# Kernel optimization log

Measured on AMD Instinct MI355X. Metric: run time of the kernel, lower is better.

The kernel has to match this reference:

```python
import jax, jax.numpy as jnp
import numpy as np


def setup_inputs() -> dict:
    key = jax.random.key(0)
    k1, k2, k3, k4, k5 = jax.random.split(key, 5)
    B, L, G, DG = 2, 8192, 256, 8
    D = G * DG
    x1 = jax.random.normal(k1, (B, L, G, DG), dtype=jnp.float32)
    x2 = jax.random.normal(k2, (B, L, G, DG), dtype=jnp.float32)
    v = jax.random.normal(k3, (B, L, G, DG), dtype=jnp.float32)
    # implicit/explicit filter output: one length-L kernel per group, scaled down
    # like a decaying long-conv filter so outputs stay O(1)
    t = jnp.arange(L, dtype=jnp.float32)
    decay = jnp.exp(-t / 1024.0)[None, :]  # (1, L)
    h = jax.random.normal(k4, (G, L), dtype=jnp.float32) * decay / jnp.sqrt(jnp.float32(L))
    conv_bias = jax.random.normal(k5, (D,), dtype=jnp.float32)
    return {"x1": x1, "x2": x2, "v": v, "h": h, "conv_bias": conv_bias}


def reference(x1, x2, v, h, conv_bias):
    # x1, x2, v: (B, L, G, DG); h: (G, L); conv_bias: (G*DG,)
    B, L, G, DG = x1.shape
    D = G * DG
    # 'b l g dg -> b (g dg) l'
    x1c = x1.reshape(B, L, D).transpose(0, 2, 1)  # (B, D, L)
    x2c = x2.reshape(B, L, D).transpose(0, 2, 1)
    vc = v.reshape(B, L, D).transpose(0, 2, 1)

    kv = x2c * vc  # pre-gate: (B, D, L)

    fft_size = 2 * L  # causal (linear) convolution via zero-padded FFT
    # each group's filter is shared across its DG channels
    h_rep = jnp.repeat(h, DG, axis=0)  # (D, L)
    kv_f = jnp.fft.rfft(kv.astype(jnp.float32), n=fft_size)
    h_f = jnp.fft.rfft(h_rep.astype(jnp.float32), n=fft_size)
    y = jnp.fft.irfft(kv_f * h_f[None], n=fft_size)[..., :L]  # (B, D, L)

    y = y + kv * conv_bias[None, :, None]  # skip/bias term
    z = x1c * y  # post-gate (identity gating activation)

    # back to (B, L, D)
    return z.transpose(0, 2, 1)
```

## Files before the change

kernel.cpp:

```cpp
#include <hip/hip_runtime.h>
#include <hip/hip_bf16.h>

typedef __attribute__((ext_vector_type(8))) __bf16 bf16x8;
typedef __attribute__((ext_vector_type(4))) __bf16 bf16x4;
typedef __attribute__((ext_vector_type(4))) float  f32x4;

#define L_LEN   8192
#define D_DIM   2048
#define G_NUM   256
#define HP      8320
#define HS      808
#define KVS     264

__global__ __launch_bounds__(256) void prep_kv_kernel(
    const float* __restrict__ x2, const float* __restrict__ v,
    __bf16* __restrict__ kvout)
{
  __shared__ __bf16 sT[128 * 64];
  const int tid = threadIdx.x;
  const int l0 = blockIdx.x << 7;
  const int d0 = blockIdx.y << 6;
  const int b  = blockIdx.z;
  const int lr = tid >> 4;
  const int dq = tid & 15;
#pragma unroll
  for (int p = 0; p < 8; ++p) {
    const int ll = (p << 4) + lr;
    const size_t idx = ((size_t)(b * L_LEN + l0 + ll)) * D_DIM + d0 + (dq << 2);
    const f32x4 a = *(const f32x4*)&x2[idx];
    const f32x4 c = *(const f32x4*)&v[idx];
    bf16x4 kvv;
    kvv[0] = (__bf16)(a[0] * c[0]);
    kvv[1] = (__bf16)(a[1] * c[1]);
    kvv[2] = (__bf16)(a[2] * c[2]);
    kvv[3] = (__bf16)(a[3] * c[3]);
    *(bf16x4*)&sT[(ll << 6) + (((dq ^ (ll >> 3)) & 15) << 2)] = kvv;
  }
  __syncthreads();
#pragma unroll
  for (int p = 0; p < 2; ++p) {
    const int c  = tid + (p << 8);
    const int r  = c >> 3, seg = c & 7;
    const int rb = r >> 2, rl = r & 3;
    const int gch = d0 + r;
    const int row = ((gch >> 3) << 4) + (b << 3) + (gch & 7);
    bf16x8 w0, w1;
#pragma unroll
    for (int j = 0; j < 8; ++j) {
      const int lj0 = (seg << 4) + j;
      const int lj1 = lj0 + 8;
      w0[j] = sT[(lj0 << 6) + (((rb ^ (lj0 >> 3)) & 15) << 2) + rl];
      w1[j] = sT[(lj1 << 6) + (((rb ^ (lj1 >> 3)) & 15) << 2) + rl];
    }
    __bf16* dst = kvout + (size_t)row * L_LEN + l0 + (seg << 4);
    *(bf16x8*)dst = w0;
    *(bf16x8*)(dst + 8) = w1;
  }
}

__global__ __launch_bounds__(256) void prep_h_kernel(
    const float* __restrict__ h, __bf16* __restrict__ hr)
{
  const unsigned i = blockIdx.x * 256u + threadIdx.x;
  const unsigned g = i / (8u * HP);
  const unsigned r = i - g * (8u * HP);
  const unsigned s = r / HP;
  const unsigned z = r - s * HP;
  const int P = 8255 - (int)z - (int)s;
  __bf16 val = (__bf16)0.0f;
  if (P >= 0 && P < 8192) val = (__bf16)h[(size_t)g * 8192 + P];
  hr[i] = val;
}

__global__ __launch_bounds__(256, 3) void conv_kernel(
    const __bf16* __restrict__ KV, const __bf16* __restrict__ HR,
    const float* __restrict__ x1, const float* __restrict__ bias,
    float* __restrict__ out)
{
  __shared__ __bf16 sKV[2][16 * KVS];
  __shared__ __bf16 sH[2][8 * HS];

  const int g   = blockIdx.x;
  const int jb  = 15 - (int)blockIdx.y;
  const int l0  = jb << 9;
  const int tid = threadIdx.x;
  const int lane = tid & 63, wv = tid >> 6;
  const int m = lane & 15, q = lane >> 4;

  const __bf16* __restrict__ KVg = KV + (size_t)g * (16 * L_LEN);
  const __bf16* __restrict__ HRg = HR + (size_t)g * (8 * HP);

  f32x4 acc0 = {0.f,0.f,0.f,0.f}, acc1 = acc0, acc2 = acc0, acc3 = acc0,
        acc4 = acc0, acc5 = acc0, acc6 = acc0, acc7 = acc0;

  bf16x8 zed;
#pragma unroll
  for (int k = 0; k < 8; ++k) zed[k] = (__bf16)0.0f;

  const int cst = tid >> 4, tst = (tid & 15) << 3;
  const int s_c   = (7 - m) & 7;
  const int bbase = m * KVS + (q << 3);
  const int wend  = l0 + (wv << 7) + 128;

  const int u0 = tid, u1 = tid + 256, u2 = tid + 512, u3 = tid + 768;
  const int sh0 = u0 / 98, sh1 = u1 / 98, sh2 = u2 / 98, sh3 = u3 / 98;
  const int o0 = (u0 - sh0 * 98) << 3, o1 = (u1 - sh1 * 98) << 3;
  const int o2 = (u2 - sh2 * 98) << 3, o3 = (u3 - sh3 * 98) << 3;
  const int w0 = sh0 * HS + o0, w1 = sh1 * HS + o1;
  const int w2 = sh2 * HS + o2, w3 = sh3 * HS + o3;
  const bool vld3 = (u3 < 8 * 98);

  const int nt = (l0 + 512) >> 8;

  bf16x8 pkv0, pkv1, ph0, ph1, ph2, ph3;

#define STAGE_LOAD(tbn) do {                                                     \
    const int Bvn = 8255 - l0 + (tbn);                                           \
    const int Y0n = (Bvn - 518) & ~7;                                            \
    pkv0 = *(const bf16x8*)&KVg[cst * L_LEN + (tbn) + tst];                      \
    pkv1 = *(const bf16x8*)&KVg[cst * L_LEN + (tbn) + tst + 128];                \
    int yy;                                                                      \
    yy = Y0n + o0; ph0 = (yy + 8 <= HP) ? *(const bf16x8*)&HRg[sh0 * HP + yy] : zed; \
    yy = Y0n + o1; ph1 = (yy + 8 <= HP) ? *(const bf16x8*)&HRg[sh1 * HP + yy] : zed; \
    yy = Y0n + o2; ph2 = (yy + 8 <= HP) ? *(const bf16x8*)&HRg[sh2 * HP + yy] : zed; \
    yy = Y0n + o3; ph3 = (vld3 && yy + 8 <= HP) ? *(const bf16x8*)&HRg[sh3 * HP + yy] : zed; \
  } while (0)

#define STAGE_WRITE(bi) do {                                                     \
    *(bf16x8*)&sKV[bi][cst * KVS + tst]       = pkv0;                            \
    *(bf16x8*)&sKV[bi][cst * KVS + tst + 128] = pkv1;                            \
    *(bf16x8*)&sH[bi][w0] = ph0;                                                 \
    *(bf16x8*)&sH[bi][w1] = ph1;                                                 \
    *(bf16x8*)&sH[bi][w2] = ph2;                                                 \
    if (vld3) *(bf16x8*)&sH[bi][w3] = ph3;                                       \
  } while (0)

  STAGE_LOAD(0);
  STAGE_WRITE(0);
  __syncthreads();

  int cur = 0;
  for (int t = 0; t < nt; ++t) {
    const int tb = t << 8;
    const bool pf = (t + 1 < nt);
    if (pf) STAGE_LOAD(tb + 256);

    if (tb < wend) {
      const __bf16* __restrict__ sHc  = sH[cur];
      const __bf16* __restrict__ sKVc = sKV[cur];
      const int Bv = 8255 - l0 + tb;
      const int Y0 = (Bv - 518) & ~7;
      const int zbase = Bv - (wv << 7) - m + (q << 3);
      const int abase = s_c * HS + (zbase - s_c - Y0) - 112;

#define AFR(f) (*(const bf16x8*)&sHc[abase + ((f) << 4)])
#define BFR(j) (*(const bf16x8*)&sKVc[bbase + ((j) << 5)])
#define MF(ac, ar) ac = __builtin_amdgcn_mfma_f32_16x16x32_bf16(ar, bq, ac, 0, 0, 0)
      bf16x8 a0=AFR(0),a1=AFR(1),a2=AFR(2),a3=AFR(3),a4=AFR(4),a5=AFR(5),a6=AFR(6),a7=AFR(7);
      bf16x8 bq;
      bq = BFR(0);
      MF(acc0,a7); MF(acc1,a6); MF(acc2,a5); MF(acc3,a4); MF(acc4,a3); MF(acc5,a2); MF(acc6,a1); MF(acc7,a0);
      a0 = AFR(8);  a1 = AFR(9);  bq = BFR(1);
      MF(acc0,a1); MF(acc1,a0); MF(acc2,a7); MF(acc3,a6); MF(acc4,a5); MF(acc5,a4); MF(acc6,a3); MF(acc7,a2);
      a2 = AFR(10); a3 = AFR(11); bq = BFR(2);
      MF(acc0,a3); MF(acc1,a2); MF(acc2,a1); MF(acc3,a0); MF(acc4,a7); MF(acc5,a6); MF(acc6,a5); MF(acc7,a4);
      a4 = AFR(12); a5 = AFR(13); bq = BFR(3);
      MF(acc0,a5); MF(acc1,a4); MF(acc2,a3); MF(acc3,a2); MF(acc4,a1); MF(acc5,a0); MF(acc6,a7); MF(acc7,a6);
      a6 = AFR(14); a7 = AFR(15); bq = BFR(4);
      MF(acc0,a7); MF(acc1,a6); MF(acc2,a5); MF(acc3,a4); MF(acc4,a3); MF(acc5,a2); MF(acc6,a1); MF(acc7,a0);
      a0 = AFR(16); a1 = AFR(17); bq = BFR(5);
      MF(acc0,a1); MF(acc1,a0); MF(acc2,a7); MF(acc3,a6); MF(acc4,a5); MF(acc5,a4); MF(acc6,a3); MF(acc7,a2);
      a2 = AFR(18); a3 = AFR(19); bq = BFR(6);
      MF(acc0,a3); MF(acc1,a2); MF(acc2,a1); MF(acc3,a0); MF(acc4,a7); MF(acc5,a6); MF(acc6,a5); MF(acc7,a4);
      a4 = AFR(20); a5 = AFR(21); bq = BFR(7);
      MF(acc0,a5); MF(acc1,a4); MF(acc2,a3); MF(acc3,a2); MF(acc4,a1); MF(acc5,a0); MF(acc6,a7); MF(acc7,a6);
#undef MF
#undef BFR
#undef AFR
    }

    if (pf) STAGE_WRITE(cur ^ 1);
    __syncthreads();
    cur ^= 1;
  }
#undef STAGE_LOAD
#undef STAGE_WRITE

  const int c = m;
  const int bb = c >> 3, dg = c & 7;
  const float bv = bias[(g << 3) + dg];

#define CONV_EPI(i, accv) {                                                     \
    const int l = l0 + (wv << 7) + ((i) << 4) + (q << 2);                       \
    const bf16x4 kv4 = *(const bf16x4*)&KVg[c * L_LEN + l];                     \
    for (int r = 0; r < 4; ++r) {                                               \
      const float y = accv[r] + (float)kv4[r] * bv;                             \
      const size_t oidx = ((size_t)(bb * L_LEN + l + r)) * D_DIM + (g << 3) + dg;\
      out[oidx] = x1[oidx] * y;                                                 \
    } }

  CONV_EPI(0, acc0)
  CONV_EPI(1, acc1)
  CONV_EPI(2, acc2)
  CONV_EPI(3, acc3)
  CONV_EPI(4, acc4)
  CONV_EPI(5, acc5)
  CONV_EPI(6, acc6)
  CONV_EPI(7, acc7)
#undef CONV_EPI
}

extern "C" void kernel_launch(void* const* d_in, const int* in_sizes, int n_in,
                              void* d_out, int out_size, void* d_ws, size_t ws_size,
                              hipStream_t stream)
{
  const float* x1 = (const float*)d_in[0];
  const float* x2 = (const float*)d_in[1];
  const float* v  = (const float*)d_in[2];
  const float* h  = (const float*)d_in[3];
  const float* cb = (const float*)d_in[4];
  float* out = (float*)d_out;

  __bf16* kv = (__bf16*)d_ws;
  __bf16* hr = kv + (size_t)G_NUM * 16 * L_LEN;

  prep_kv_kernel<<<dim3(L_LEN / 128, D_DIM / 64, 2), 256, 0, stream>>>(x2, v, kv);
  prep_h_kernel<<<(G_NUM * 8 * HP) / 256, 256, 0, stream>>>(h, hr);
  conv_kernel<<<dim3(G_NUM, 16), 256, 0, stream>>>(kv, hr, x1, cb, out);
}
```

Baseline: 694.3 us.

## Double output tile per block and stream filter through shared-memory ring buffer

Each conv block now computes 1024 output positions (16 accumulators per wave) instead of 512, which halves the number of blocks and doubles the reuse of each loaded KV/filter fragment across MFMAs. The per-step filter window is replaced by a 2048-entry circular buffer in shared memory, so each step loads only one new 256-wide slice of the Toeplitz filter instead of reloading the full window. Block indices are remapped so that consecutive groups land on the same XCD. In exchange, register pressure rises (occupancy hint drops from 3 to 2), the grid is smaller, and the causal triangular load imbalance between blocks grows.

```diff
diff --git a/kernel.cpp b/kernel.cpp
--- a/kernel.cpp
+++ b/kernel.cpp
@@ -9,8 +9,10 @@
 #define D_DIM   2048
 #define G_NUM   256
 #define HP      8320
-#define HS      808
 #define KVS     264
+#define HRING   2048
+#define HMSK    2047
+#define HSTR    2088
 
 __global__ __launch_bounds__(256) void prep_kv_kernel(
     const float* __restrict__ x2, const float* __restrict__ v,
@@ -72,17 +74,19 @@
   hr[i] = val;
 }
 
-__global__ __launch_bounds__(256, 3) void conv_kernel(
+__global__ __launch_bounds__(256, 2) void conv_kernel(
     const __bf16* __restrict__ KV, const __bf16* __restrict__ HR,
     const float* __restrict__ x1, const float* __restrict__ bias,
     float* __restrict__ out)
 {
-  __shared__ __bf16 sKV[2][16 * KVS];
-  __shared__ __bf16 sH[2][8 * HS];
-
-  const int g   = blockIdx.x;
-  const int jb  = 15 - (int)blockIdx.y;
-  const int l0  = jb << 9;
+  __shared__ __align__(16) __bf16 sKV[2][16 * KVS];
+  __shared__ __align__(16) __bf16 sH[8 * HSTR];
+
+  const int n   = blockIdx.x;
+  const int xcd = n & 7, k = n >> 3;
+  const int g   = ((k >> 3) << 3) | xcd;
+  const int jb  = 7 - (k & 7);
+  const int l0  = jb << 10;
   const int tid = threadIdx.x;
   const int lane = tid & 63, wv = tid >> 6;
   const int m = lane & 15, q = lane >> 4;
@@ -90,108 +94,108 @@
   const __bf16* __restrict__ KVg = KV + (size_t)g * (16 * L_LEN);
   const __bf16* __restrict__ HRg = HR + (size_t)g * (8 * HP);
 
-  f32x4 acc0 = {0.f,0.f,0.f,0.f}, acc1 = acc0, acc2 = acc0, acc3 = acc0,
-        acc4 = acc0, acc5 = acc0, acc6 = acc0, acc7 = acc0;
+  f32x4 z4 = {0.f,0.f,0.f,0.f};
+  f32x4 c0=z4,c1=z4,c2=z4,c3=z4,c4=z4,c5=z4,c6=z4,c7=z4,
+        c8=z4,c9=z4,c10=z4,c11=z4,c12=z4,c13=z4,c14=z4,c15=z4;
 
   bf16x8 zed;
 #pragma unroll
-  for (int k = 0; k < 8; ++k) zed[k] = (__bf16)0.0f;
+  for (int kk = 0; kk < 8; ++kk) zed[kk] = (__bf16)0.0f;
 
   const int cst = tid >> 4, tst = (tid & 15) << 3;
   const int s_c   = (7 - m) & 7;
   const int bbase = m * KVS + (q << 3);
-  const int wend  = l0 + (wv << 7) + 128;
-
-  const int u0 = tid, u1 = tid + 256, u2 = tid + 512, u3 = tid + 768;
-  const int sh0 = u0 / 98, sh1 = u1 / 98, sh2 = u2 / 98, sh3 = u3 / 98;
-  const int o0 = (u0 - sh0 * 98) << 3, o1 = (u1 - sh1 * 98) << 3;
-  const int o2 = (u2 - sh2 * 98) << 3, o3 = (u3 - sh3 * 98) << 3;
-  const int w0 = sh0 * HS + o0, w1 = sh1 * HS + o1;
-  const int w2 = sh2 * HS + o2, w3 = sh3 * HS + o3;
-  const bool vld3 = (u3 < 8 * 98);
-
-  const int nt = (l0 + 512) >> 8;
-
-  bf16x8 pkv0, pkv1, ph0, ph1, ph2, ph3;
-
-#define STAGE_LOAD(tbn) do {                                                     \
-    const int Bvn = 8255 - l0 + (tbn);                                           \
-    const int Y0n = (Bvn - 518) & ~7;                                            \
-    pkv0 = *(const bf16x8*)&KVg[cst * L_LEN + (tbn) + tst];                      \
-    pkv1 = *(const bf16x8*)&KVg[cst * L_LEN + (tbn) + tst + 128];                \
-    int yy;                                                                      \
-    yy = Y0n + o0; ph0 = (yy + 8 <= HP) ? *(const bf16x8*)&HRg[sh0 * HP + yy] : zed; \
-    yy = Y0n + o1; ph1 = (yy + 8 <= HP) ? *(const bf16x8*)&HRg[sh1 * HP + yy] : zed; \
-    yy = Y0n + o2; ph2 = (yy + 8 <= HP) ? *(const bf16x8*)&HRg[sh2 * HP + yy] : zed; \
-    yy = Y0n + o3; ph3 = (vld3 && yy + 8 <= HP) ? *(const bf16x8*)&HRg[sh3 * HP + yy] : zed; \
-  } while (0)
-
-#define STAGE_WRITE(bi) do {                                                     \
-    *(bf16x8*)&sKV[bi][cst * KVS + tst]       = pkv0;                            \
-    *(bf16x8*)&sKV[bi][cst * KVS + tst + 128] = pkv1;                            \
-    *(bf16x8*)&sH[bi][w0] = ph0;                                                 \
-    *(bf16x8*)&sH[bi][w1] = ph1;                                                 \
-    *(bf16x8*)&sH[bi][w2] = ph2;                                                 \
-    if (vld3) *(bf16x8*)&sH[bi][w3] = ph3;                                       \
-  } while (0)
-
-  STAGE_LOAD(0);
-  STAGE_WRITE(0);
+  const int wend  = l0 + (wv << 8) + 256;
+  const int hs_s  = tid >> 5;
+  const int hs_c  = (tid & 31) << 3;
+  const int hwb   = hs_s * HSTR;
+
+  const int nt = (l0 + 1024) >> 8;
+
+  {
+    *(bf16x8*)&sKV[0][cst * KVS + tst]       = *(const bf16x8*)&KVg[cst * L_LEN + tst];
+    *(bf16x8*)&sKV[0][cst * KVS + tst + 128] = *(const bf16x8*)&KVg[cst * L_LEN + tst + 128];
+    const int YB0 = 7232 - l0;
+    for (int s = 0; s < 8; ++s) {
+      for (int cc = tid; cc < 159; cc += 256) {
+        const int y = YB0 + (cc << 3);
+        bf16x8 w = (y + 8 <= HP) ? *(const bf16x8*)&HRg[s * HP + y] : zed;
+        *(bf16x8*)&sH[s * HSTR + (y & HMSK)] = w;
+      }
+    }
+  }
   __syncthreads();
 
   int cur = 0;
+  bf16x8 pkv0, pkv1, ph;
+  int py = 0;
   for (int t = 0; t < nt; ++t) {
     const int tb = t << 8;
     const bool pf = (t + 1 < nt);
-    if (pf) STAGE_LOAD(tb + 256);
+    if (pf) {
+      const int tbn = tb + 256;
+      pkv0 = *(const bf16x8*)&KVg[cst * L_LEN + tbn + tst];
+      pkv1 = *(const bf16x8*)&KVg[cst * L_LEN + tbn + tst + 128];
+      py = 8504 - l0 + tb + hs_c;
+      ph = (py + 8 <= HP) ? *(const bf16x8*)&HRg[hs_s * HP + py] : zed;
+    }
 
     if (tb < wend) {
-      const __bf16* __restrict__ sHc  = sH[cur];
       const __bf16* __restrict__ sKVc = sKV[cur];
+      const __bf16* __restrict__ sHc  = sH + s_c * HSTR;
       const int Bv = 8255 - l0 + tb;
-      const int Y0 = (Bv - 518) & ~7;
-      const int zbase = Bv - (wv << 7) - m + (q << 3);
-      const int abase = s_c * HS + (zbase - s_c - Y0) - 112;
-
-#define AFR(f) (*(const bf16x8*)&sHc[abase + ((f) << 4)])
+      const int ybase = Bv - (wv << 8) - m + (q << 3) - s_c - 240;
+
+#define AFR(f) (*(const bf16x8*)&sHc[(ybase + ((f) << 4)) & HMSK])
 #define BFR(j) (*(const bf16x8*)&sKVc[bbase + ((j) << 5)])
 #define MF(ac, ar) ac = __builtin_amdgcn_mfma_f32_16x16x32_bf16(ar, bq, ac, 0, 0, 0)
-      bf16x8 a0=AFR(0),a1=AFR(1),a2=AFR(2),a3=AFR(3),a4=AFR(4),a5=AFR(5),a6=AFR(6),a7=AFR(7);
+      bf16x8 t0=AFR(0),t1=AFR(1),t2=AFR(2),t3=AFR(3),t4=AFR(4),t5=AFR(5),t6=AFR(6),t7=AFR(7),
+             t8=AFR(8),t9=AFR(9),t10=AFR(10),t11=AFR(11),t12=AFR(12),t13=AFR(13),t14=AFR(14),t15=AFR(15);
       bf16x8 bq;
       bq = BFR(0);
-      MF(acc0,a7); MF(acc1,a6); MF(acc2,a5); MF(acc3,a4); MF(acc4,a3); MF(acc5,a2); MF(acc6,a1); MF(acc7,a0);
-      a0 = AFR(8);  a1 = AFR(9);  bq = BFR(1);
-      MF(acc0,a1); MF(acc1,a0); MF(acc2,a7); MF(acc3,a6); MF(acc4,a5); MF(acc5,a4); MF(acc6,a3); MF(acc7,a2);
-      a2 = AFR(10); a3 = AFR(11); bq = BFR(2);
-      MF(acc0,a3); MF(acc1,a2); MF(acc2,a1); MF(acc3,a0); MF(acc4,a7); MF(acc5,a6); MF(acc6,a5); MF(acc7,a4);
-      a4 = AFR(12); a5 = AFR(13); bq = BFR(3);
-      MF(acc0,a5); MF(acc1,a4); MF(acc2,a3); MF(acc3,a2); MF(acc4,a1); MF(acc5,a0); MF(acc6,a7); MF(acc7,a6);
-      a6 = AFR(14); a7 = AFR(15); bq = BFR(4);
-      MF(acc0,a7); MF(acc1,a6); MF(acc2,a5); MF(acc3,a4); MF(acc4,a3); MF(acc5,a2); MF(acc6,a1); MF(acc7,a0);
-      a0 = AFR(16); a1 = AFR(17); bq = BFR(5);
-      MF(acc0,a1); MF(acc1,a0); MF(acc2,a7); MF(acc3,a6); MF(acc4,a5); MF(acc5,a4); MF(acc6,a3); MF(acc7,a2);
-      a2 = AFR(18); a3 = AFR(19); bq = BFR(6);
-      MF(acc0,a3); MF(acc1,a2); MF(acc2,a1); MF(acc3,a0); MF(acc4,a7); MF(acc5,a6); MF(acc6,a5); MF(acc7,a4);
-      a4 = AFR(20); a5 = AFR(21); bq = BFR(7);
-      MF(acc0,a5); MF(acc1,a4); MF(acc2,a3); MF(acc3,a2); MF(acc4,a1); MF(acc5,a0); MF(acc6,a7); MF(acc7,a6);
+      MF(c0,t15); MF(c1,t14); MF(c2,t13); MF(c3,t12); MF(c4,t11); MF(c5,t10); MF(c6,t9); MF(c7,t8);
+      MF(c8,t7); MF(c9,t6); MF(c10,t5); MF(c11,t4); MF(c12,t3); MF(c13,t2); MF(c14,t1); MF(c15,t0);
+      t0 = AFR(16); t1 = AFR(17); bq = BFR(1);
+      MF(c0,t1); MF(c1,t0); MF(c2,t15); MF(c3,t14); MF(c4,t13); MF(c5,t12); MF(c6,t11); MF(c7,t10);
+      MF(c8,t9); MF(c9,t8); MF(c10,t7); MF(c11,t6); MF(c12,t5); MF(c13,t4); MF(c14,t3); MF(c15,t2);
+      t2 = AFR(18); t3 = AFR(19); bq = BFR(2);
+      MF(c0,t3); MF(c1,t2); MF(c2,t1); MF(c3,t0); MF(c4,t15); MF(c5,t14); MF(c6,t13); MF(c7,t12);
+      MF(c8,t11); MF(c9,t10); MF(c10,t9); MF(c11,t8); MF(c12,t7); MF(c13,t6); MF(c14,t5); MF(c15,t4);
+      t4 = AFR(20); t5 = AFR(21); bq = BFR(3);
+      MF(c0,t5); MF(c1,t4); MF(c2,t3); MF(c3,t2); MF(c4,t1); MF(c5,t0); MF(c6,t15); MF(c7,t14);
+      MF(c8,t13); MF(c9,t12); MF(c10,t11); MF(c11,t10); MF(c12,t9); MF(c13,t8); MF(c14,t7); MF(c15,t6);
+      t6 = AFR(22); t7 = AFR(23); bq = BFR(4);
+      MF(c0,t7); MF(c1,t6); MF(c2,t5); MF(c3,t4); MF(c4,t3); MF(c5,t2); MF(c6,t1); MF(c7,t0);
+      MF(c8,t15); MF(c9,t14); MF(c10,t13); MF(c11,t12); MF(c12,t11); MF(c13,t10); MF(c14,t9); MF(c15,t8);
+      t8 = AFR(24); t9 = AFR(25); bq = BFR(5);
+      MF(c0,t9); MF(c1,t8); MF(c2,t7); MF(c3,t6); MF(c4,t5); MF(c5,t4); MF(c6,t3); MF(c7,t2);
+      MF(c8,t1); MF(c9,t0); MF(c10,t15); MF(c11,t14); MF(c12,t13); MF(c13,t12); MF(c14,t11); MF(c15,t10);
+      t10 = AFR(26); t11 = AFR(27); bq = BFR(6);
+      MF(c0,t11); MF(c1,t10); MF(c2,t9); MF(c3,t8); MF(c4,t7); MF(c5,t6); MF(c6,t5); MF(c7,t4);
+      MF(c8,t3); MF(c9,t2); MF(c10,t1); MF(c11,t0); MF(c12,t15); MF(c13,t14); MF(c14,t13); MF(c15,t12);
+      t12 = AFR(28); t13 = AFR(29); bq = BFR(7);
+      MF(c0,t13); MF(c1,t12); MF(c2,t11); MF(c3,t10); MF(c4,t9); MF(c5,t8); MF(c6,t7); MF(c7,t6);
+      MF(c8,t5); MF(c9,t4); MF(c10,t3); MF(c11,t2); MF(c12,t1); MF(c13,t0); MF(c14,t15); MF(c15,t14);
 #undef MF
 #undef BFR
 #undef AFR
     }
 
-    if (pf) STAGE_WRITE(cur ^ 1);
+    if (pf) {
+      *(bf16x8*)&sKV[cur ^ 1][cst * KVS + tst]       = pkv0;
+      *(bf16x8*)&sKV[cur ^ 1][cst * KVS + tst + 128] = pkv1;
+      *(bf16x8*)&sH[hwb + (py & HMSK)] = ph;
+    }
     __syncthreads();
     cur ^= 1;
   }
-#undef STAGE_LOAD
-#undef STAGE_WRITE
 
   const int c = m;
   const int bb = c >> 3, dg = c & 7;
   const float bv = bias[(g << 3) + dg];
 
 #define CONV_EPI(i, accv) {                                                     \
-    const int l = l0 + (wv << 7) + ((i) << 4) + (q << 2);                       \
+    const int l = l0 + (wv << 8) + ((i) << 4) + (q << 2);                       \
     const bf16x4 kv4 = *(const bf16x4*)&KVg[c * L_LEN + l];                     \
     for (int r = 0; r < 4; ++r) {                                               \
       const float y = accv[r] + (float)kv4[r] * bv;                             \
@@ -199,14 +203,10 @@
       out[oidx] = x1[oidx] * y;                                                 \
     } }
 
-  CONV_EPI(0, acc0)
-  CONV_EPI(1, acc1)
-  CONV_EPI(2, acc2)
-  CONV_EPI(3, acc3)
-  CONV_EPI(4, acc4)
-  CONV_EPI(5, acc5)
-  CONV_EPI(6, acc6)
-  CONV_EPI(7, acc7)
+  CONV_EPI(0,  c0)  CONV_EPI(1,  c1)  CONV_EPI(2,  c2)  CONV_EPI(3,  c3)
+  CONV_EPI(4,  c4)  CONV_EPI(5,  c5)  CONV_EPI(6,  c6)  CONV_EPI(7,  c7)
+  CONV_EPI(8,  c8)  CONV_EPI(9,  c9)  CONV_EPI(10, c10) CONV_EPI(11, c11)
+  CONV_EPI(12, c12) CONV_EPI(13, c13) CONV_EPI(14, c14) CONV_EPI(15, c15)
 #undef CONV_EPI
 }
 
@@ -226,5 +226,5 @@
 
   prep_kv_kernel<<<dim3(L_LEN / 128, D_DIM / 64, 2), 256, 0, stream>>>(x2, v, kv);
   prep_h_kernel<<<(G_NUM * 8 * HP) / 256, 256, 0, stream>>>(h, hr);
-  conv_kernel<<<dim3(G_NUM, 16), 256, 0, stream>>>(kv, hr, x1, cb, out);
-}
+  conv_kernel<<<2048, 256, 0, stream>>>(kv, hr, x1, cb, out);
+}
```

New measurement: 724.5 us. 4.4% more time.
